# Kernel optimization log

Measured on AMD Instinct MI355X. Metric: run time of the kernel, lower is better.

## Reference

```python
import jax, jax.numpy as jnp
import numpy as np

N_NODES = 50000
N_EDGES = 800000
IN_CH = 256
OUT_CH = 128


def setup_inputs() -> dict:
    key = jax.random.key(0)
    k1, k2, k3, k4, k5, k6 = jax.random.split(key, 6)
    x = jax.random.normal(k1, (N_NODES, IN_CH), dtype=jnp.float32)
    edge_rows = jax.random.randint(k2, (N_EDGES,), 0, N_NODES, dtype=jnp.int64)
    edge_cols = jax.random.randint(k3, (N_EDGES,), 0, N_NODES, dtype=jnp.int64)
    # positive edge weights, roughly like a normalized adjacency (~1/degree)
    edge_vals = jax.random.uniform(k4, (N_EDGES,), dtype=jnp.float32) / 16.0
    # xavier_uniform: bound = sqrt(6/(fan_in+fan_out))
    bound = float(np.sqrt(6.0 / (IN_CH + OUT_CH)))
    weight = jax.random.uniform(k5, (IN_CH, OUT_CH), dtype=jnp.float32, minval=-bound, maxval=bound)
    gate_weight = jax.random.uniform(k6, (IN_CH, OUT_CH), dtype=jnp.float32, minval=-bound, maxval=bound)
    return {"x": x, "edge_rows": edge_rows, "edge_cols": edge_cols,
            "edge_vals": edge_vals, "weight": weight, "gate_weight": gate_weight}


def _spmm(edge_rows, edge_cols, edge_vals, dense, n_rows):
    # out[r] = sum over edges (r, c, v): v * dense[c]
    gathered = edge_vals[:, None] * dense[edge_cols]  # [E, out_ch]
    return jax.ops.segment_sum(gathered, edge_rows, num_segments=n_rows)


def reference(x, edge_rows, edge_cols, edge_vals, weight, gate_weight):
    support = x @ weight          # [N, out_ch]
    gate = x @ gate_weight        # [N, out_ch]
    n = x.shape[0]
    agg_support = _spmm(edge_rows, edge_cols, edge_vals, support, n)
    agg_gate = _spmm(edge_rows, edge_cols, edge_vals, gate, n)
    return jax.nn.sigmoid(agg_gate) * agg_support
```

## Files before the change

kernel.cpp:

```cpp
#include <hip/hip_runtime.h>
#include <hip/hip_bf16.h>

#define IN_CH 256
#define OUT_CH 128
#define NCAT 256
#define CAP 64
#define RPB 128
#define BINCAP 3072
#define EPB 4096

typedef __attribute__((ext_vector_type(8))) short bf16x8;
typedef __attribute__((ext_vector_type(4))) float f32x4;

__device__ __forceinline__ unsigned short f2bf(float f) {
  unsigned int u = __builtin_bit_cast(unsigned int, f);
  u += 0x7FFFu + ((u >> 16) & 1u);
  return (unsigned short)(u >> 16);
}
__device__ __forceinline__ unsigned int pack2bf(float a, float b) {
  return (unsigned int)f2bf(a) | ((unsigned int)f2bf(b) << 16);
}
__device__ __forceinline__ float bflo(unsigned int u) {
  return __builtin_bit_cast(float, u << 16);
}
__device__ __forceinline__ float bfhi(unsigned int u) {
  return __builtin_bit_cast(float, u & 0xFFFF0000u);
}

__global__ __launch_bounds__(256) void init_wcat(
    const float* __restrict__ w, const float* __restrict__ gw,
    unsigned short* __restrict__ wcatT, int* __restrict__ coarse_cnt,
    int nbins) {
  const int b = blockIdx.x;
  if (b < 256) {
    const int c = b;
    const int k = threadIdx.x;
    const float v = (c < 128) ? w[(size_t)k * 128 + c]
                              : gw[(size_t)k * 128 + (c - 128)];
    wcatT[(size_t)c * 256 + k] = f2bf(v);
  } else {
    for (int j = threadIdx.x; j < nbins; j += 256) coarse_cnt[j] = 0;
  }
}

#define BM 128
#define AST 528

__global__ __launch_bounds__(512) void gemm_and_bin(
    const float* __restrict__ x, const unsigned short* __restrict__ wcatT,
    char* __restrict__ comb, int nrows,
    const int* __restrict__ er, const int* __restrict__ ec,
    const float* __restrict__ ev, int* __restrict__ coarse_cnt,
    unsigned* __restrict__ cA, unsigned char* __restrict__ cB,
    int E, int nbins, int binBlocks) {
  __shared__ char smem[BM * AST];

  if (blockIdx.x < binBlocks) {
    int* scnt = (int*)smem;
    int* sbase = (int*)smem + 512;
    const int t = threadIdx.x;
    const int e0 = blockIdx.x * EPB;

    if (t < 512) scnt[t] = 0;
    __syncthreads();

    int myr[8];
#pragma unroll
    for (int i = 0; i < 8; ++i) {
      const int e = e0 + i * 512 + t;
      int r = -1;
      if (e < E) { r = er[e]; atomicAdd(&scnt[r >> 7], 1); }
      myr[i] = r;
    }
    __syncthreads();

    if (t < nbins)
      sbase[t] = (scnt[t] > 0) ? atomicAdd(&coarse_cnt[t], scnt[t]) : 0;
    __syncthreads();
    if (t < 512) scnt[t] = 0;
    __syncthreads();

#pragma unroll
    for (int i = 0; i < 8; ++i) {
      const int r = myr[i];
      if (r >= 0) {
        const int e = e0 + i * 512 + t;
        const int b = r >> 7;
        const int idx = sbase[b] + atomicAdd(&scnt[b], 1);
        if (idx < BINCAP) {
          const size_t g = (size_t)b * BINCAP + idx;
          cA[g] = ((unsigned)ec[e] << 16) | (unsigned)f2bf(ev[e]);
          cB[g] = (unsigned char)(r & (RPB - 1));
        }
      }
    }
    return;
  }

  const int t = threadIdx.x;
  const int lane = t & 63;
  const int wv = t >> 6;
  const int wr = wv >> 2;
  const int wc = wv & 3;
  const int blockRow = (blockIdx.x - binBlocks) * BM;
  const int lrow = lane & 15;
  const int klane = lane >> 4;

  {
    const int arow = t >> 2;
    const int aseg = t & 3;
    const int agrow = blockRow + arow;
    const bool aok = (agrow < nrows);
    const float* src = x + (size_t)agrow * IN_CH + aseg * 64;
    char* dst = smem + arow * AST + aseg * 128;
#pragma unroll
    for (int g = 0; g < 4; ++g) {
      float4 v0 = make_float4(0, 0, 0, 0), v1 = v0, v2 = v0, v3 = v0;
      if (aok) {
        v0 = *(const float4*)(src + g * 16 + 0);
        v1 = *(const float4*)(src + g * 16 + 4);
        v2 = *(const float4*)(src + g * 16 + 8);
        v3 = *(const float4*)(src + g * 16 + 12);
      }
      uint4 pk0, pk1;
      pk0.x = pack2bf(v0.x, v0.y); pk0.y = pack2bf(v0.z, v0.w);
      pk0.z = pack2bf(v1.x, v1.y); pk0.w = pack2bf(v1.z, v1.w);
      pk1.x = pack2bf(v2.x, v2.y); pk1.y = pack2bf(v2.z, v2.w);
      pk1.z = pack2bf(v3.x, v3.y); pk1.w = pack2bf(v3.z, v3.w);
      *(uint4*)(dst + g * 32 + 0)  = pk0;
      *(uint4*)(dst + g * 32 + 16) = pk1;
    }
  }
  __syncthreads();

  f32x4 acc[4][4];
#pragma unroll
  for (int m = 0; m < 4; ++m)
#pragma unroll
    for (int n = 0; n < 4; ++n) acc[m][n] = (f32x4){0.f, 0.f, 0.f, 0.f};

  const char* bbase = (const char*)wcatT + (size_t)(wc * 64 + lrow) * 512 + klane * 16;

#pragma unroll
  for (int kk = 0; kk < 8; ++kk) {
    bf16x8 af[4], bfr[4];
#pragma unroll
    for (int m = 0; m < 4; ++m)
      af[m] = *(const bf16x8*)(smem + (wr * 64 + m * 16 + lrow) * AST + kk * 64 + klane * 16);
#pragma unroll
    for (int n = 0; n < 4; ++n)
      bfr[n] = *(const bf16x8*)(bbase + (size_t)n * 16 * 512 + kk * 64);
#pragma unroll
    for (int m = 0; m < 4; ++m)
#pragma unroll
      for (int n = 0; n < 4; ++n)
        acc[m][n] = __builtin_amdgcn_mfma_f32_16x16x32_bf16(af[m], bfr[n], acc[m][n], 0, 0, 0);
  }
  __syncthreads();

#pragma unroll
  for (int h = 0; h < 2; ++h) {
    if (wr == h) {
#pragma unroll
      for (int m = 0; m < 4; ++m) {
#pragma unroll
        for (int n = 0; n < 4; ++n) {
#pragma unroll
          for (int j = 0; j < 4; ++j) {
            const int rl = m * 16 + klane * 4 + j;
            const int gcol = wc * 64 + n * 16 + lrow;
            const int ch = gcol & 127;
            const int isg = gcol >> 7;
            const int byteoff = (ch >> 1) * 8 + isg * 4 + (ch & 1) * 2;
            *(unsigned short*)(smem + rl * 512 + byteoff) = f2bf(acc[m][n][j]);
          }
        }
      }
    }
    __syncthreads();
#pragma unroll
    for (int it = 0; it < 4; ++it) {
      const int lin = it * 512 + t;
      const int rl = lin >> 5;
      const int grow = blockRow + h * 64 + rl;
      if (grow < nrows)
        *(float4*)(comb + (size_t)grow * 512 + (lin & 31) * 16) =
            *(const float4*)(smem + lin * 16);
    }
    __syncthreads();
  }
}

__global__ __launch_bounds__(256) void bin_fine(
    const int* __restrict__ coarse_cnt, const unsigned* __restrict__ cA,
    const unsigned char* __restrict__ cB, int* __restrict__ cnt,
    unsigned* __restrict__ bucket4, int nrows) {
  __shared__ unsigned fine[RPB * CAP];
  __shared__ int lcnt[RPB];
  const int t = threadIdx.x;
  const int b = blockIdx.x;
  const int r0 = b * RPB;

  for (int j = t; j < RPB; j += 256) lcnt[j] = 0;
  __syncthreads();

  const int nE = min(coarse_cnt[b], BINCAP);
  for (int i = t; i < nE; i += 256) {
    const unsigned a = cA[(size_t)b * BINCAP + i];
    const int rl = cB[(size_t)b * BINCAP + i];
    const int idx = atomicAdd(&lcnt[rl], 1);
    if (idx < CAP) fine[rl * CAP + idx] = a;
  }
  __syncthreads();

  if (t < RPB && r0 + t < nrows) cnt[r0 + t] = min(lcnt[t], CAP);

  for (int s = t; s < RPB * CAP; s += 256) {
    const int rl = s >> 6;
    const int sl = s & 63;
    if (sl < min(lcnt[rl], CAP) && r0 + rl < nrows)
      bucket4[(size_t)(r0 + rl) * CAP + sl] = fine[s];
  }
}

__global__ __launch_bounds__(256) void spmm_fused(
    const unsigned* __restrict__ bucket4, const int* __restrict__ cnt,
    const char* __restrict__ comb, float* __restrict__ out, int nrows) {
  const int wid = (int)((blockIdx.x * 256 + threadIdx.x) >> 6);
  const int lane = threadIdx.x & 63;
  if (wid >= nrows) return;

  const int deg = min(cnt[wid], CAP);
  float s0 = 0.f, s1 = 0.f, g0 = 0.f, g1 = 0.f;

  if (deg > 0) {
    const unsigned my = bucket4[(size_t)wid * CAP + lane];
    for (int d = 0; d < deg; d += 8) {
      unsigned cj[8]; float vj[8]; uint2 q[8];
#pragma unroll
      for (int j = 0; j < 8; ++j) {
        const int dj = d + j;
        const int ds = dj < deg ? dj : deg - 1;
        const unsigned ent = (unsigned)__shfl((int)my, ds);
        cj[j] = ent >> 16;
        vj[j] = (dj < deg) ? bflo(ent) : 0.f;
      }
#pragma unroll
      for (int j = 0; j < 8; ++j)
        q[j] = *(const uint2*)(comb + (size_t)cj[j] * 512 + lane * 8);
#pragma unroll
      for (int j = 0; j < 8; ++j) {
        s0 += vj[j] * bflo(q[j].x);  s1 += vj[j] * bfhi(q[j].x);
        g0 += vj[j] * bflo(q[j].y);  g1 += vj[j] * bfhi(q[j].y);
      }
    }
  }
  const float o0 = s0 / (1.f + __expf(-g0));
  const float o1 = s1 / (1.f + __expf(-g1));
  *(float2*)&out[(size_t)wid * OUT_CH + lane * 2] = make_float2(o0, o1);
}

extern "C" void kernel_launch(void* const* d_in, const int* in_sizes, int n_in,
                              void* d_out, int out_size, void* d_ws, size_t ws_size,
                              hipStream_t stream) {
  const float* x  = (const float*)d_in[0];
  const int*   er = (const int*)d_in[1];
  const int*   ec = (const int*)d_in[2];
  const float* ev = (const float*)d_in[3];
  const float* w  = (const float*)d_in[4];
  const float* gw = (const float*)d_in[5];
  float* out = (float*)d_out;

  const int N = in_sizes[0] / IN_CH;
  const int E = in_sizes[1];
  const int nbins = (N + RPB - 1) / RPB;

  char* ws = (char*)d_ws;
  char* comb = ws;
  size_t off = (size_t)N * 512;
  unsigned short* wcatT = (unsigned short*)(ws + off);  off += 256 * 256 * 2;
  int* cnt = (int*)(ws + off);                          off += ((size_t)N * 4 + 255) & ~255ull;
  unsigned* bucket4 = (unsigned*)(ws + off);            off += (size_t)N * CAP * 4;
  int* coarse_cnt = (int*)(ws + off);                   off += ((size_t)nbins * 4 + 255) & ~255ull;
  unsigned* cA = (unsigned*)(ws + off);                 off += (size_t)nbins * BINCAP * 4;
  unsigned char* cB = (unsigned char*)(ws + off);

  init_wcat<<<257, 256, 0, stream>>>(w, gw, wcatT, coarse_cnt, nbins);

  const int binBlocks = (E + EPB - 1) / EPB;
  const int gemmBlocks = (N + BM - 1) / BM;
  gemm_and_bin<<<binBlocks + gemmBlocks, 512, 0, stream>>>(
      x, wcatT, comb, N, er, ec, ev, coarse_cnt, cA, cB, E, nbins, binBlocks);

  bin_fine<<<nbins, 256, 0, stream>>>(coarse_cnt, cA, cB, cnt, bucket4, N);

  const int blocks = (N + 3) / 4;
  spmm_fused<<<blocks, 256, 0, stream>>>(bucket4, cnt, comb, out, N);
}
```

Baseline: 119.3 us.

## Load GEMM A-fragments straight to registers and write comb directly from accumulators

The fused GEMM now uses 256-thread blocks where each wave owns 16 rows and all 256 output columns. It loads x straight into MFMA A-fragment registers instead of staging through a 67KB LDS tile. Results are packed and stored from accumulators into the comb buffer in a permuted channel layout, with no LDS transpose. spmm_fused is adjusted to match that layout with scattered scalar output stores. The goal is to cut LDS use and barriers and raise occupancy. In exchange, B fragments are no longer shared across waves (more global/L2 reads of wcatT) and the stores are less coalesced.

```diff
diff --git a/kernel.cpp b/kernel.cpp
--- a/kernel.cpp
+++ b/kernel.cpp
@@ -43,48 +43,45 @@
   }
 }
 
-#define BM 128
-#define AST 528
-
-__global__ __launch_bounds__(512) void gemm_and_bin(
+__global__ __launch_bounds__(256) void gemm_and_bin(
     const float* __restrict__ x, const unsigned short* __restrict__ wcatT,
     char* __restrict__ comb, int nrows,
     const int* __restrict__ er, const int* __restrict__ ec,
     const float* __restrict__ ev, int* __restrict__ coarse_cnt,
     unsigned* __restrict__ cA, unsigned char* __restrict__ cB,
     int E, int nbins, int binBlocks) {
-  __shared__ char smem[BM * AST];
+  __shared__ int sh[1024];
 
   if (blockIdx.x < binBlocks) {
-    int* scnt = (int*)smem;
-    int* sbase = (int*)smem + 512;
+    int* scnt = sh;
+    int* sbase = sh + 512;
     const int t = threadIdx.x;
     const int e0 = blockIdx.x * EPB;
 
-    if (t < 512) scnt[t] = 0;
-    __syncthreads();
-
-    int myr[8];
-#pragma unroll
-    for (int i = 0; i < 8; ++i) {
-      const int e = e0 + i * 512 + t;
+    for (int j = t; j < 512; j += 256) scnt[j] = 0;
+    __syncthreads();
+
+    int myr[16];
+#pragma unroll
+    for (int i = 0; i < 16; ++i) {
+      const int e = e0 + i * 256 + t;
       int r = -1;
       if (e < E) { r = er[e]; atomicAdd(&scnt[r >> 7], 1); }
       myr[i] = r;
     }
     __syncthreads();
 
-    if (t < nbins)
-      sbase[t] = (scnt[t] > 0) ? atomicAdd(&coarse_cnt[t], scnt[t]) : 0;
-    __syncthreads();
-    if (t < 512) scnt[t] = 0;
-    __syncthreads();
-
-#pragma unroll
-    for (int i = 0; i < 8; ++i) {
+    for (int j = t; j < nbins; j += 256)
+      sbase[j] = (scnt[j] > 0) ? atomicAdd(&coarse_cnt[j], scnt[j]) : 0;
+    __syncthreads();
+    for (int j = t; j < 512; j += 256) scnt[j] = 0;
+    __syncthreads();
+
+#pragma unroll
+    for (int i = 0; i < 16; ++i) {
       const int r = myr[i];
       if (r >= 0) {
-        const int e = e0 + i * 512 + t;
+        const int e = e0 + i * 256 + t;
         const int b = r >> 7;
         const int idx = sbase[b] + atomicAdd(&scnt[b], 1);
         if (idx < BINCAP) {
@@ -100,94 +97,61 @@
   const int t = threadIdx.x;
   const int lane = t & 63;
   const int wv = t >> 6;
-  const int wr = wv >> 2;
-  const int wc = wv & 3;
-  const int blockRow = (blockIdx.x - binBlocks) * BM;
   const int lrow = lane & 15;
   const int klane = lane >> 4;
-
+  const int r0 = (blockIdx.x - binBlocks) * 64 + wv * 16;
+  const int myrow = r0 + lrow;
+  const bool rok = (myrow < nrows);
+
+  bf16x8 af[8];
   {
-    const int arow = t >> 2;
-    const int aseg = t & 3;
-    const int agrow = blockRow + arow;
-    const bool aok = (agrow < nrows);
-    const float* src = x + (size_t)agrow * IN_CH + aseg * 64;
-    char* dst = smem + arow * AST + aseg * 128;
-#pragma unroll
-    for (int g = 0; g < 4; ++g) {
-      float4 v0 = make_float4(0, 0, 0, 0), v1 = v0, v2 = v0, v3 = v0;
-      if (aok) {
-        v0 = *(const float4*)(src + g * 16 + 0);
-        v1 = *(const float4*)(src + g * 16 + 4);
-        v2 = *(const float4*)(src + g * 16 + 8);
-        v3 = *(const float4*)(src + g * 16 + 12);
-      }
-      uint4 pk0, pk1;
-      pk0.x = pack2bf(v0.x, v0.y); pk0.y = pack2bf(v0.z, v0.w);
-      pk0.z = pack2bf(v1.x, v1.y); pk0.w = pack2bf(v1.z, v1.w);
-      pk1.x = pack2bf(v2.x, v2.y); pk1.y = pack2bf(v2.z, v2.w);
-      pk1.z = pack2bf(v3.x, v3.y); pk1.w = pack2bf(v3.z, v3.w);
-      *(uint4*)(dst + g * 32 + 0)  = pk0;
-      *(uint4*)(dst + g * 32 + 16) = pk1;
-    }
-  }
-  __syncthreads();
-
-  f32x4 acc[4][4];
-#pragma unroll
-  for (int m = 0; m < 4; ++m)
-#pragma unroll
-    for (int n = 0; n < 4; ++n) acc[m][n] = (f32x4){0.f, 0.f, 0.f, 0.f};
-
-  const char* bbase = (const char*)wcatT + (size_t)(wc * 64 + lrow) * 512 + klane * 16;
-
-#pragma unroll
-  for (int kk = 0; kk < 8; ++kk) {
-    bf16x8 af[4], bfr[4];
-#pragma unroll
-    for (int m = 0; m < 4; ++m)
-      af[m] = *(const bf16x8*)(smem + (wr * 64 + m * 16 + lrow) * AST + kk * 64 + klane * 16);
-#pragma unroll
-    for (int n = 0; n < 4; ++n)
-      bfr[n] = *(const bf16x8*)(bbase + (size_t)n * 16 * 512 + kk * 64);
-#pragma unroll
-    for (int m = 0; m < 4; ++m)
-#pragma unroll
-      for (int n = 0; n < 4; ++n)
-        acc[m][n] = __builtin_amdgcn_mfma_f32_16x16x32_bf16(af[m], bfr[n], acc[m][n], 0, 0, 0);
-  }
-  __syncthreads();
-
-#pragma unroll
-  for (int h = 0; h < 2; ++h) {
-    if (wr == h) {
-#pragma unroll
-      for (int m = 0; m < 4; ++m) {
-#pragma unroll
-        for (int n = 0; n < 4; ++n) {
-#pragma unroll
-          for (int j = 0; j < 4; ++j) {
-            const int rl = m * 16 + klane * 4 + j;
-            const int gcol = wc * 64 + n * 16 + lrow;
-            const int ch = gcol & 127;
-            const int isg = gcol >> 7;
-            const int byteoff = (ch >> 1) * 8 + isg * 4 + (ch & 1) * 2;
-            *(unsigned short*)(smem + rl * 512 + byteoff) = f2bf(acc[m][n][j]);
-          }
-        }
-      }
-    }
-    __syncthreads();
-#pragma unroll
-    for (int it = 0; it < 4; ++it) {
-      const int lin = it * 512 + t;
-      const int rl = lin >> 5;
-      const int grow = blockRow + h * 64 + rl;
-      if (grow < nrows)
-        *(float4*)(comb + (size_t)grow * 512 + (lin & 31) * 16) =
-            *(const float4*)(smem + lin * 16);
-    }
-    __syncthreads();
+    const float* xr = x + (size_t)myrow * IN_CH + klane * 8;
+#pragma unroll
+    for (int kk = 0; kk < 8; ++kk) {
+      float4 v0 = make_float4(0, 0, 0, 0), v1 = v0;
+      if (rok) {
+        v0 = *(const float4*)(xr + kk * 32);
+        v1 = *(const float4*)(xr + kk * 32 + 4);
+      }
+      uint4 pk;
+      pk.x = pack2bf(v0.x, v0.y); pk.y = pack2bf(v0.z, v0.w);
+      pk.z = pack2bf(v1.x, v1.y); pk.w = pack2bf(v1.z, v1.w);
+      af[kk] = __builtin_bit_cast(bf16x8, pk);
+    }
+  }
+
+  f32x4 acc[16];
+#pragma unroll
+  for (int n = 0; n < 16; ++n) acc[n] = (f32x4){0.f, 0.f, 0.f, 0.f};
+
+  const char* bbase = (const char*)wcatT + (size_t)lrow * 512 + klane * 16;
+#pragma unroll
+  for (int half = 0; half < 2; ++half) {
+#pragma unroll
+    for (int kk = 0; kk < 8; ++kk) {
+      bf16x8 bfr[8];
+#pragma unroll
+      for (int n = 0; n < 8; ++n)
+        bfr[n] = *(const bf16x8*)(bbase + (size_t)(half * 8 + n) * 16 * 512 + kk * 64);
+#pragma unroll
+      for (int n = 0; n < 8; ++n)
+        acc[half * 8 + n] =
+            __builtin_amdgcn_mfma_f32_16x16x32_bf16(af[kk], bfr[n], acc[half * 8 + n], 0, 0, 0);
+    }
+  }
+
+#pragma unroll
+  for (int gg = 0; gg < 4; ++gg) {
+#pragma unroll
+    for (int j = 0; j < 4; ++j) {
+      const int grow = r0 + klane * 4 + j;
+      if (grow < nrows) {
+        uint2 val;
+        val.x = pack2bf(acc[2 * gg][j],     acc[2 * gg + 8][j]);
+        val.y = pack2bf(acc[2 * gg + 1][j], acc[2 * gg + 9][j]);
+        *(uint2*)(comb + (size_t)grow * 512 + gg * 128 + lrow * 8) = val;
+      }
+    }
   }
 }
 
@@ -231,7 +195,7 @@
   if (wid >= nrows) return;
 
   const int deg = min(cnt[wid], CAP);
-  float s0 = 0.f, s1 = 0.f, g0 = 0.f, g1 = 0.f;
+  float s1 = 0.f, g1 = 0.f, s2 = 0.f, g2 = 0.f;
 
   if (deg > 0) {
     const unsigned my = bucket4[(size_t)wid * CAP + lane];
@@ -250,14 +214,17 @@
         q[j] = *(const uint2*)(comb + (size_t)cj[j] * 512 + lane * 8);
 #pragma unroll
       for (int j = 0; j < 8; ++j) {
-        s0 += vj[j] * bflo(q[j].x);  s1 += vj[j] * bfhi(q[j].x);
-        g0 += vj[j] * bflo(q[j].y);  g1 += vj[j] * bfhi(q[j].y);
-      }
-    }
-  }
-  const float o0 = s0 / (1.f + __expf(-g0));
+        s1 += vj[j] * bflo(q[j].x);  g1 += vj[j] * bfhi(q[j].x);
+        s2 += vj[j] * bflo(q[j].y);  g2 += vj[j] * bfhi(q[j].y);
+      }
+    }
+  }
+  const int gg = lane >> 4, lr = lane & 15;
+  const int c1 = 32 * gg + lr;
   const float o1 = s1 / (1.f + __expf(-g1));
-  *(float2*)&out[(size_t)wid * OUT_CH + lane * 2] = make_float2(o0, o1);
+  const float o2 = s2 / (1.f + __expf(-g2));
+  out[(size_t)wid * OUT_CH + c1]      = o1;
+  out[(size_t)wid * OUT_CH + c1 + 16] = o2;
 }
 
 extern "C" void kernel_launch(void* const* d_in, const int* in_sizes, int n_in,
@@ -288,8 +255,8 @@
   init_wcat<<<257, 256, 0, stream>>>(w, gw, wcatT, coarse_cnt, nbins);
 
   const int binBlocks = (E + EPB - 1) / EPB;
-  const int gemmBlocks = (N + BM - 1) / BM;
-  gemm_and_bin<<<binBlocks + gemmBlocks, 512, 0, stream>>>(
+  const int gemmBlocks = (N + 63) / 64;
+  gemm_and_bin<<<binBlocks + gemmBlocks, 256, 0, stream>>>(
       x, wcatT, comb, N, er, ec, ev, coarse_cnt, cA, cB, E, nbins, binBlocks);
 
   bin_fine<<<nbins, 256, 0, stream>>>(coarse_cnt, cA, cB, cnt, bucket4, N);
```

New measurement: 143.8 us. +20.6%, slower.
